# Kernel tuning notes

Measured on AMD Instinct MI355X. Metric: run time of the kernel, lower is better.

Reference implementation:

```python
import jax, jax.numpy as jnp
import numpy as np

N_DIM = 32
N_HEADS = 4
HEAD_SIZE = N_DIM // N_HEADS  # 8


def setup_inputs() -> dict:
    key = jax.random.key(0)
    ks = jax.random.split(key, 9)
    B, T = 16, 2048
    s = 1.0 / np.sqrt(N_DIM)
    inp = {
        "x": jax.random.normal(ks[0], (B, T, N_DIM), dtype=jnp.float32),
        "Wq": jax.random.uniform(ks[1], (N_DIM, N_DIM), jnp.float32, -s, s),
        "bq": jax.random.uniform(ks[2], (N_DIM,), jnp.float32, -s, s),
        "Wk": jax.random.uniform(ks[3], (N_DIM, N_DIM), jnp.float32, -s, s),
        "bk": jax.random.uniform(ks[4], (N_DIM,), jnp.float32, -s, s),
        "Wv": jax.random.uniform(ks[5], (N_DIM, N_DIM), jnp.float32, -s, s),
        "bv": jax.random.uniform(ks[6], (N_DIM,), jnp.float32, -s, s),
        "Wp": jax.random.uniform(ks[7], (N_DIM, N_DIM), jnp.float32, -s, s),
        "bp": jax.random.uniform(ks[8], (N_DIM,), jnp.float32, -s, s),
    }
    return inp


def reference(x, Wq, bq, Wk, bk, Wv, bv, Wp, bp):
    b, t, c = x.shape
    # nn.Linear: y = x @ W^T + b
    def heads(W, bias):
        y = jnp.einsum("btc,dc->btd", x, W) + bias
        return y.reshape(b, t, N_HEADS, HEAD_SIZE).transpose(0, 2, 1, 3)  # [b,h,t,d]

    q = heads(Wq, bq)
    k = heads(Wk, bk)
    v = heads(Wv, bv)

    scores = jnp.einsum("bhqd,bhkd->bhqk", q, k) / np.sqrt(HEAD_SIZE)  # [b,h,t,t]
    causal = jnp.tril(jnp.ones((t, t), dtype=bool))
    scores = jnp.where(causal[None, None], scores, -jnp.inf)
    weights = jax.nn.softmax(scores, axis=-1)
    # dropout layers are identity in eval mode
    z = jnp.einsum("bhqk,bhkd->bhqd", weights, v)
    z = z.transpose(0, 2, 1, 3).reshape(b, t, N_DIM)
    z = jnp.einsum("btc,dc->btd", z, Wp) + bp
    return z
```

## Files before the change

kernel.cpp:

```cpp
#include <hip/hip_runtime.h>
#include <math.h>

#define BB 16
#define TT 2048
#define CC 32
#define HH 4
#define DD 8

#define KBS 2056
#define VRS 264
#define VBS (9 * VRS)
#define ZP 33

typedef __fp16 h2  __attribute__((ext_vector_type(2)));
typedef __fp16 h8  __attribute__((ext_vector_type(8)));
typedef float  fx16 __attribute__((ext_vector_type(16)));
typedef int    i4v __attribute__((ext_vector_type(4)));
typedef int    i2v __attribute__((ext_vector_type(2)));

__device__ __forceinline__ h2 pkh(float a, float b) {
#if __has_builtin(__builtin_amdgcn_cvt_pkrtz)
    return __builtin_amdgcn_cvt_pkrtz(a, b);
#else
    h2 r; r.x = (__fp16)a; r.y = (__fp16)b; return r;
#endif
}

__device__ __forceinline__ float fexp2(float x) {
#if __has_builtin(__builtin_amdgcn_exp2f)
    return __builtin_amdgcn_exp2f(x);
#else
    return exp2f(x);
#endif
}

__device__ __forceinline__ int h2bits(h2 v) { return __builtin_bit_cast(int, v); }

__device__ __forceinline__ void makeP(const fx16& S, bool last, int thr, int hi, h8* P) {
    float pe[16];
    #pragma unroll
    for (int r = 0; r < 16; r++) {
        const int ko = (r & 3) + 8 * (r >> 2);
        float sv = S[r];
        if (last) sv = (ko <= thr) ? sv : -INFINITY;
        pe[r] = fexp2(sv);
    }
    int Hh[8];
    #pragma unroll
    for (int i = 0; i < 8; i++) Hh[i] = h2bits(pkh(pe[2*i], pe[2*i+1]));
#if __has_builtin(__builtin_amdgcn_permlane32_swap)
    #pragma unroll
    for (int s = 0; s < 2; s++) {
        const int b0 = 4 * s;
        auto ra = __builtin_amdgcn_permlane32_swap(Hh[b0+0], Hh[b0+2], false, false);
        auto rb = __builtin_amdgcn_permlane32_swap(Hh[b0+1], Hh[b0+3], false, false);
        i2v pa = __builtin_bit_cast(i2v, ra);
        i2v pb = __builtin_bit_cast(i2v, rb);
        i4v f;
        f.x = pa.x; f.y = pb.x; f.z = pa.y; f.w = pb.y;
        P[s] = __builtin_bit_cast(h8, f);
    }
#else
    #pragma unroll
    for (int s = 0; s < 2; s++) {
        const int b0 = 4 * s;
        int own0 = hi ? Hh[b0+2] : Hh[b0+0];
        int own1 = hi ? Hh[b0+3] : Hh[b0+1];
        int snd0 = hi ? Hh[b0+0] : Hh[b0+2];
        int snd1 = hi ? Hh[b0+1] : Hh[b0+3];
        int rcv0 = __shfl_xor(snd0, 32);
        int rcv1 = __shfl_xor(snd1, 32);
        i4v f;
        f.x = hi ? rcv0 : own0;
        f.y = hi ? rcv1 : own1;
        f.z = hi ? own0 : rcv0;
        f.w = hi ? own1 : rcv1;
        P[s] = __builtin_bit_cast(h8, f);
    }
#endif
}

__global__ __launch_bounds__(256) void qkv_kernel(
    const float* __restrict__ x,
    const float* __restrict__ Wq, const float* __restrict__ bq,
    const float* __restrict__ Wk, const float* __restrict__ bk,
    const float* __restrict__ Wv, const float* __restrict__ bv,
    __fp16* __restrict__ Qo, __fp16* __restrict__ Ko, __fp16* __restrict__ Vo)
{
    __shared__ float Xs[256 * ZP];
    const int tid = threadIdx.x;
    const int h = blockIdx.y;
    const int row0 = blockIdx.x * 256;

    {
        const float4* xg = (const float4*)(x + (size_t)row0 * CC);
        #pragma unroll
        for (int i = 0; i < 8; i++) {
            const int idx = tid + 256 * i;
            float4 f = xg[idx];
            const int w = idx * 4;
            float* d = &Xs[(w >> 5) * ZP + (w & 31)];
            d[0] = f.x; d[1] = f.y; d[2] = f.z; d[3] = f.w;
        }
    }
    __syncthreads();

    const int row = row0 + tid;
    const int b = row >> 11, t = row & 2047;
    const int bh = b * HH + h;

    float xr[CC];
    #pragma unroll
    for (int c = 0; c < CC; c++) xr[c] = Xs[tid * ZP + c];

    {
        float o[DD];
        #pragma unroll
        for (int d = 0; d < DD; d++) {
            const int dd = h * DD + d;
            float acc = bq[dd];
            #pragma unroll
            for (int c = 0; c < CC; c++) acc += xr[c] * Wq[dd * CC + c];
            o[d] = acc;
        }
        const float qs = 0.3535533905932738f * 1.4426950408889634f;
        i4v qw;
        qw.x = h2bits(pkh(o[0]*qs, o[1]*qs)); qw.y = h2bits(pkh(o[2]*qs, o[3]*qs));
        qw.z = h2bits(pkh(o[4]*qs, o[5]*qs)); qw.w = h2bits(pkh(o[6]*qs, o[7]*qs));
        *(i4v*)(Qo + ((size_t)bh * TT + t) * DD) = qw;
    }
    {
        float o[DD];
        #pragma unroll
        for (int d = 0; d < DD; d++) {
            const int dd = h * DD + d;
            float acc = bk[dd];
            #pragma unroll
            for (int c = 0; c < CC; c++) acc += xr[c] * Wk[dd * CC + c];
            o[d] = acc;
        }
        i4v kw;
        kw.x = h2bits(pkh(o[0], o[1])); kw.y = h2bits(pkh(o[2], o[3]));
        kw.z = h2bits(pkh(o[4], o[5])); kw.w = h2bits(pkh(o[6], o[7]));
        *(i4v*)(Ko + ((size_t)bh * TT + t) * DD) = kw;
    }
    {
        float o[DD];
        #pragma unroll
        for (int d = 0; d < DD; d++) {
            const int dd = h * DD + d;
            float acc = bv[dd];
            #pragma unroll
            for (int c = 0; c < CC; c++) acc += xr[c] * Wv[dd * CC + c];
            o[d] = acc;
        }
        __fp16* vt = Vo + (size_t)bh * 9 * TT + t;
        #pragma unroll
        for (int d = 0; d < DD; d++) vt[d * TT] = (__fp16)o[d];
        vt[8 * TT] = (__fp16)1.0f;
    }
}

__global__ __launch_bounds__(512, 4) void attn_kernel(
    const __fp16* __restrict__ Qg, const __fp16* __restrict__ Kg,
    const __fp16* __restrict__ Vg,
    const float* __restrict__ Wp, const float* __restrict__ bp,
    float* __restrict__ out)
{
    __shared__ __align__(16) __fp16 KsS[4 * KBS];
    __shared__ __align__(16) __fp16 VtS[4 * VBS];
    __shared__ float zbuf[64 * ZP];

    const int tid  = threadIdx.x;
    const int b    = blockIdx.x & 15;
    const int ip   = blockIdx.x >> 4;
    const int w    = tid >> 6;
    const int h    = w & 3;
    const int qsel = w >> 2;
    const int lane = tid & 63;
    const int qc   = lane & 31;
    const int hi   = lane >> 5;

    const int bh  = b * HH + h;
    const int qb  = 32 * (qsel ? (63 - ip) : ip);
    const int keys_needed = qb + 32;
    const int nstBlk = (32 * (63 - ip) + 32 + 255) >> 8;

    h8 qf;
    {
        h8 qz;
        #pragma unroll
        for (int i = 0; i < 8; i++) qz[i] = (__fp16)0.0f;
        h8 qa = *(const h8*)(Qg + ((size_t)bh * TT + qb + qc) * DD);
        qf = hi ? qz : qa;
    }

    fx16 O, zc;
    #pragma unroll
    for (int i = 0; i < 16; i++) { O[i] = 0.0f; zc[i] = 0.0f; }

    const int vrow = (qc < 9) ? qc : 8;
    const int thr  = qc - 4 * hi;

    const __fp16* kgl = Kg + (size_t)bh * TT * DD;
    const __fp16* vgl = Vg + (size_t)bh * 9 * TT;
    __fp16* kld = KsS + h * KBS;
    __fp16* vld = VtS + h * VBS;
    const __fp16* kb = kld + qc * DD;
    const __fp16* vb = vld + vrow * VRS + 8 * hi;

    i4v kpre[4], vpre[5];
    if (qsel) {
        const i4v* ks = (const i4v*)kgl;
        #pragma unroll
        for (int r = 0; r < 4; r++) kpre[r] = ks[lane + 64 * r];
        #pragma unroll
        for (int r = 0; r < 5; r++) {
            int i = lane + 64 * r; if (i > 287) i = 287;
            vpre[r] = *(const i4v*)(vgl + (i >> 5) * TT + (i & 31) * 8);
        }
    }

    for (int sti = 0; sti < nstBlk; sti++) {
        const int st = sti * 256;
        if (qsel) {
            i4v* kd = (i4v*)kld;
            #pragma unroll
            for (int r = 0; r < 4; r++) kd[lane + 64 * r] = kpre[r];
            #pragma unroll
            for (int r = 0; r < 5; r++) {
                const int i = lane + 64 * r;
                if (i < 288) *(i4v*)(vld + (i >> 5) * VRS + (i & 31) * 8) = vpre[r];
            }
            if (sti + 1 < nstBlk) {
                const int st2 = st + 256;
                const i4v* ks = (const i4v*)(kgl + (size_t)st2 * DD);
                #pragma unroll
                for (int r = 0; r < 4; r++) kpre[r] = ks[lane + 64 * r];
                #pragma unroll
                for (int r = 0; r < 5; r++) {
                    int i = lane + 64 * r; if (i > 287) i = 287;
                    vpre[r] = *(const i4v*)(vgl + (i >> 5) * TT + st2 + (i & 31) * 8);
                }
            }
        }
        __syncthreads();

        const int kend = min(st + 256, keys_needed);
        for (int kt = st; kt < kend; kt += 32) {
            h8 kf = *(const h8*)(kb + (kt - st) * DD);
            fx16 S = __builtin_amdgcn_mfma_f32_32x32x16_f16(kf, qf, zc, 0, 0, 0);
            h8 P[2];
            makeP(S, kt == qb, thr, hi, P);
            #pragma unroll
            for (int s = 0; s < 2; s++) {
                h8 vf = *(const h8*)(vb + (kt - st) + 16 * s);
                O = __builtin_amdgcn_mfma_f32_32x32x16_f16(vf, P[s], O, 0, 0, 0);
            }
        }
        __syncthreads();
    }

    {
        const float inv = 1.0f / O[4];
        float* z = &zbuf[(qsel * 32 + qc) * ZP + h * DD + 4 * hi];
        z[0] = O[0]*inv; z[1] = O[1]*inv; z[2] = O[2]*inv; z[3] = O[3]*inv;
    }
    __syncthreads();

    {
        const int seg = tid >> 6;
        const int r = tid & 63;
        float zr[CC];
        #pragma unroll
        for (int c = 0; c < CC; c++) zr[c] = zbuf[r * ZP + c];
        float o[4];
        #pragma unroll
        for (int d = 0; d < 4; d++) {
            const int dd = seg * 4 + d;
            float acc = bp[dd];
            #pragma unroll
            for (int c = 0; c < CC; c++) acc += zr[c] * Wp[dd * CC + c];
            o[d] = acc;
        }
        const int qglob = (r < 32) ? (ip * 32 + r) : ((63 - ip) * 32 + (r - 32));
        float* dst = out + ((size_t)b * TT + qglob) * CC + seg * 4;
        *(float4*)dst = make_float4(o[0], o[1], o[2], o[3]);
    }
}

extern "C" void kernel_launch(void* const* d_in, const int* in_sizes, int n_in,
                              void* d_out, int out_size, void* d_ws, size_t ws_size,
                              hipStream_t stream) {
    const float* x  = (const float*)d_in[0];
    const float* Wq = (const float*)d_in[1];
    const float* bq = (const float*)d_in[2];
    const float* Wk = (const float*)d_in[3];
    const float* bk = (const float*)d_in[4];
    const float* Wv = (const float*)d_in[5];
    const float* bv = (const float*)d_in[6];
    const float* Wp = (const float*)d_in[7];
    const float* bp = (const float*)d_in[8];
    float* out = (float*)d_out;

    const size_t NE = (size_t)BB * HH * TT * DD;
    __fp16* Qh = (__fp16*)d_ws;
    __fp16* Kh = Qh + NE;
    __fp16* Vt = Kh + NE;

    qkv_kernel<<<dim3(BB * TT / 256, HH), 256, 0, stream>>>(x, Wq, bq, Wk, bk, Wv, bv, Qh, Kh, Vt);
    attn_kernel<<<dim3(BB * 32), 512, 0, stream>>>(Qh, Kh, Vt, Wp, bp, out);
}
```

Baseline: 112.9 us.

## Drop LDS staging of K/V and read fragments directly from global memory

The attention kernel no longer stages K and V tiles through shared memory with paired light/heavy query blocks. Each 256-thread block now handles one 32-query tile for all four heads, launched heaviest-first. K and V fragments are loaded straight from global memory with a one-step register prefetch. This removes the shared-memory traffic and block-wide barriers and raises the block count. The cost is more global and L2 traffic, since heads no longer share staged data across query tiles, plus causal load imbalance that is now handled only by launch order.

```diff
diff --git a/kernel.cpp b/kernel.cpp
--- a/kernel.cpp
+++ b/kernel.cpp
@@ -7,9 +7,6 @@
 #define HH 4
 #define DD 8
 
-#define KBS 2056
-#define VRS 264
-#define VBS (9 * VRS)
 #define ZP 33
 
 typedef __fp16 h2  __attribute__((ext_vector_type(2)));
@@ -161,30 +158,26 @@
     }
 }
 
-__global__ __launch_bounds__(512, 4) void attn_kernel(
+__global__ __launch_bounds__(256, 4) void attn_kernel(
     const __fp16* __restrict__ Qg, const __fp16* __restrict__ Kg,
     const __fp16* __restrict__ Vg,
     const float* __restrict__ Wp, const float* __restrict__ bp,
     float* __restrict__ out)
 {
-    __shared__ __align__(16) __fp16 KsS[4 * KBS];
-    __shared__ __align__(16) __fp16 VtS[4 * VBS];
-    __shared__ float zbuf[64 * ZP];
+    __shared__ float zbuf[32 * ZP];
 
     const int tid  = threadIdx.x;
-    const int b    = blockIdx.x & 15;
-    const int ip   = blockIdx.x >> 4;
-    const int w    = tid >> 6;
-    const int h    = w & 3;
-    const int qsel = w >> 2;
+    const int bx   = blockIdx.x;
+    const int b    = bx & 15;
+    const int qg   = 63 - (bx >> 4);
+    const int h    = tid >> 6;
     const int lane = tid & 63;
     const int qc   = lane & 31;
     const int hi   = lane >> 5;
 
     const int bh  = b * HH + h;
-    const int qb  = 32 * (qsel ? (63 - ip) : ip);
+    const int qb  = 32 * qg;
     const int keys_needed = qb + 32;
-    const int nstBlk = (32 * (63 - ip) + 32 + 255) >> 8;
 
     h8 qf;
     {
@@ -202,75 +195,38 @@
     const int vrow = (qc < 9) ? qc : 8;
     const int thr  = qc - 4 * hi;
 
-    const __fp16* kgl = Kg + (size_t)bh * TT * DD;
-    const __fp16* vgl = Vg + (size_t)bh * 9 * TT;
-    __fp16* kld = KsS + h * KBS;
-    __fp16* vld = VtS + h * VBS;
-    const __fp16* kb = kld + qc * DD;
-    const __fp16* vb = vld + vrow * VRS + 8 * hi;
-
-    i4v kpre[4], vpre[5];
-    if (qsel) {
-        const i4v* ks = (const i4v*)kgl;
-        #pragma unroll
-        for (int r = 0; r < 4; r++) kpre[r] = ks[lane + 64 * r];
-        #pragma unroll
-        for (int r = 0; r < 5; r++) {
-            int i = lane + 64 * r; if (i > 287) i = 287;
-            vpre[r] = *(const i4v*)(vgl + (i >> 5) * TT + (i & 31) * 8);
-        }
-    }
-
-    for (int sti = 0; sti < nstBlk; sti++) {
-        const int st = sti * 256;
-        if (qsel) {
-            i4v* kd = (i4v*)kld;
-            #pragma unroll
-            for (int r = 0; r < 4; r++) kd[lane + 64 * r] = kpre[r];
-            #pragma unroll
-            for (int r = 0; r < 5; r++) {
-                const int i = lane + 64 * r;
-                if (i < 288) *(i4v*)(vld + (i >> 5) * VRS + (i & 31) * 8) = vpre[r];
-            }
-            if (sti + 1 < nstBlk) {
-                const int st2 = st + 256;
-                const i4v* ks = (const i4v*)(kgl + (size_t)st2 * DD);
-                #pragma unroll
-                for (int r = 0; r < 4; r++) kpre[r] = ks[lane + 64 * r];
-                #pragma unroll
-                for (int r = 0; r < 5; r++) {
-                    int i = lane + 64 * r; if (i > 287) i = 287;
-                    vpre[r] = *(const i4v*)(vgl + (i >> 5) * TT + st2 + (i & 31) * 8);
-                }
-            }
-        }
-        __syncthreads();
-
-        const int kend = min(st + 256, keys_needed);
-        for (int kt = st; kt < kend; kt += 32) {
-            h8 kf = *(const h8*)(kb + (kt - st) * DD);
-            fx16 S = __builtin_amdgcn_mfma_f32_32x32x16_f16(kf, qf, zc, 0, 0, 0);
-            h8 P[2];
-            makeP(S, kt == qb, thr, hi, P);
-            #pragma unroll
-            for (int s = 0; s < 2; s++) {
-                h8 vf = *(const h8*)(vb + (kt - st) + 16 * s);
-                O = __builtin_amdgcn_mfma_f32_32x32x16_f16(vf, P[s], O, 0, 0, 0);
-            }
-        }
-        __syncthreads();
+    const __fp16* kgl = Kg + ((size_t)bh * TT + qc) * DD;
+    const __fp16* vgl = Vg + (size_t)bh * 9 * TT + vrow * TT + 8 * hi;
+
+    h8 kf_c  = *(const h8*)(kgl);
+    h8 vf0_c = *(const h8*)(vgl);
+    h8 vf1_c = *(const h8*)(vgl + 16);
+
+    for (int kt = 0; kt < keys_needed; kt += 32) {
+        const int ktn = (kt + 32 < keys_needed) ? kt + 32 : 0;
+        h8 kf_n  = *(const h8*)(kgl + ktn * DD);
+        h8 vf0_n = *(const h8*)(vgl + ktn);
+        h8 vf1_n = *(const h8*)(vgl + ktn + 16);
+
+        fx16 S = __builtin_amdgcn_mfma_f32_32x32x16_f16(kf_c, qf, zc, 0, 0, 0);
+        h8 P[2];
+        makeP(S, kt == qb, thr, hi, P);
+        O = __builtin_amdgcn_mfma_f32_32x32x16_f16(vf0_c, P[0], O, 0, 0, 0);
+        O = __builtin_amdgcn_mfma_f32_32x32x16_f16(vf1_c, P[1], O, 0, 0, 0);
+
+        kf_c = kf_n; vf0_c = vf0_n; vf1_c = vf1_n;
     }
 
     {
         const float inv = 1.0f / O[4];
-        float* z = &zbuf[(qsel * 32 + qc) * ZP + h * DD + 4 * hi];
+        float* z = &zbuf[qc * ZP + h * DD + 4 * hi];
         z[0] = O[0]*inv; z[1] = O[1]*inv; z[2] = O[2]*inv; z[3] = O[3]*inv;
     }
     __syncthreads();
 
     {
-        const int seg = tid >> 6;
-        const int r = tid & 63;
+        const int seg = tid >> 5;
+        const int r   = tid & 31;
         float zr[CC];
         #pragma unroll
         for (int c = 0; c < CC; c++) zr[c] = zbuf[r * ZP + c];
@@ -283,8 +239,7 @@
             for (int c = 0; c < CC; c++) acc += zr[c] * Wp[dd * CC + c];
             o[d] = acc;
         }
-        const int qglob = (r < 32) ? (ip * 32 + r) : ((63 - ip) * 32 + (r - 32));
-        float* dst = out + ((size_t)b * TT + qglob) * CC + seg * 4;
+        float* dst = out + ((size_t)b * TT + qb + r) * CC + seg * 4;
         *(float4*)dst = make_float4(o[0], o[1], o[2], o[3]);
     }
 }
@@ -309,5 +264,5 @@
     __fp16* Vt = Kh + NE;
 
     qkv_kernel<<<dim3(BB * TT / 256, HH), 256, 0, stream>>>(x, Wq, bq, Wk, bk, Wv, bv, Qh, Kh, Vt);
-    attn_kernel<<<dim3(BB * 32), 512, 0, stream>>>(Qh, Kh, Vt, Wp, bp, out);
-}
+    attn_kernel<<<dim3(BB * 64), 256, 0, stream>>>(Qh, Kh, Vt, Wp, bp, out);
+}
```

Measured after the change: 112.6 us. No clear change (-0.3%).
